# Performance work log

Hardware: AMD Instinct MI355X
Metric: run time of the kernel (lower is better)

Reference implementation:

```python
import jax, jax.numpy as jnp
import numpy as np

N = 96  # fixed by nn.LayerNorm([96]) in the module
EPS = 1e-6


def _dct2_matrix(n, dtype=jnp.float32):
    # DCT-II with the module's scaling (norm=None, returns 2*V):
    # D[k, i] = 2 * cos(pi * (2i + 1) * k / (2n))
    k = jnp.arange(n, dtype=dtype)[:, None]
    i = jnp.arange(n, dtype=dtype)[None, :]
    return 2.0 * jnp.cos(jnp.pi * (2.0 * i + 1.0) * k / (2.0 * n))


def _layernorm(y, gamma, beta):
    mu = jnp.mean(y, axis=-1, keepdims=True)
    var = jnp.mean(jnp.square(y - mu), axis=-1, keepdims=True)
    return (y - mu) * jax.lax.rsqrt(var + EPS) * gamma + beta


def setup_inputs() -> dict:
    key = jax.random.key(0)
    k1, k2, k3 = jax.random.split(key, 3)
    b, c, l = 512, 1024, N
    x = jax.random.normal(k1, (b, c, l), dtype=jnp.float32)
    # torch Linear default init ~ U(-1/sqrt(fan_in), 1/sqrt(fan_in)); gaussian*scale is fine for a baseline
    W1 = jax.random.normal(k2, (2 * N, N), dtype=jnp.float32) * (1.0 / np.sqrt(N))
    W2 = jax.random.normal(k3, (N, 2 * N), dtype=jnp.float32) * (1.0 / np.sqrt(2 * N))
    ln_gamma = jnp.ones((N,), dtype=jnp.float32)
    ln_beta = jnp.zeros((N,), dtype=jnp.float32)
    return {"x": x, "W1": W1, "W2": W2, "ln_gamma": ln_gamma, "ln_beta": ln_beta}


def reference(x, W1, W2, ln_gamma, ln_beta):
    # x: [b, c, 96]. The per-channel python loop in the original is just a
    # batched DCT-II along the last axis -> single matmul with the DCT matrix.
    D = _dct2_matrix(N, x.dtype)
    stack_dct = jnp.einsum('bcl,kl->bck', x, D)
    lr = _layernorm(stack_dct, ln_gamma, ln_beta)
    h = jax.nn.relu(jnp.einsum('bck,hk->bch', lr, W1))   # Linear(96 -> 192), dropout is identity in eval
    s = jax.nn.sigmoid(jnp.einsum('bch,kh->bck', h, W2))  # Linear(192 -> 96)
    lr_weight = _layernorm(s, ln_gamma, ln_beta)          # same LayerNorm module reused
    return x * lr_weight
```

## Files before the change

kernel.cpp:

```cpp
#include <hip/hip_runtime.h>
#include <math.h>

typedef _Float16 v8h  __attribute__((ext_vector_type(8)));
typedef float    fx4  __attribute__((ext_vector_type(4)));

#define S1_FRAGS 18
#define S2_FRAGS 36
#define S3_FRAGS 36

__global__ void prep_frags(const float* __restrict__ W1,
                           const float* __restrict__ W2,
                           v8h* __restrict__ ws) {
    const int f    = blockIdx.x;
    const int lane = threadIdx.x;
    v8h v;
    if (f < S1_FRAGS) {
        const int t = f / 3, s = f % 3;
        const int n  = t * 16 + (lane & 15);
        const int k0 = s * 32 + (lane >> 4) * 8;
#pragma unroll
        for (int j = 0; j < 8; ++j) {
            const int i = k0 + j;
            const float ang = 3.14159265358979323846f * (float)((2 * i + 1) * n) / 192.0f;
            v[j] = (_Float16)(2.0f * cosf(ang));
        }
    } else if (f < S1_FRAGS + S2_FRAGS) {
        const int g = f - S1_FRAGS;
        const int t = g / 3, s = g % 3;
        const int n  = t * 16 + (lane & 15);
        const int k0 = s * 32 + (lane >> 4) * 8;
#pragma unroll
        for (int j = 0; j < 8; ++j) v[j] = (_Float16)W1[n * 96 + k0 + j];
    } else {
        const int g = f - S1_FRAGS - S2_FRAGS;
        const int t = g / 6, s = g % 6;
        const int n  = t * 16 + (lane & 15);
        const int k0 = s * 32 + (lane >> 4) * 8;
#pragma unroll
        for (int j = 0; j < 8; ++j) v[j] = (_Float16)W2[n * 192 + k0 + j];
    }
    ws[f * 64 + lane] = v;
}

#define LDA 104
#define LDH 200

__global__ __launch_bounds__(256, 3)
void fused_dct_mlp(const float* __restrict__ x,
                   const float* __restrict__ gamma,
                   const float* __restrict__ beta,
                   const v8h* __restrict__ wf,
                   float* __restrict__ out) {
    __shared__ _Float16 LRB[64][LDA];
    __shared__ _Float16 HB[64][LDH];

    const int tid  = threadIdx.x;
    const int lane = tid & 63;
    const int wave = tid >> 6;
    const int m0   = wave * 16;
    const int lr_  = lane & 15;
    const int lk   = lane >> 4;

    const long row0 = (long)blockIdx.x * 64;
    const float* arow = x + (row0 + m0 + lr_) * 96;

    fx4 acc1[6];
#pragma unroll
    for (int t = 0; t < 6; ++t) acc1[t] = (fx4){0.f, 0.f, 0.f, 0.f};
#pragma unroll
    for (int s = 0; s < 3; ++s) {
        const float* ap = arow + s * 32 + lk * 8;
        fx4 a0 = *(const fx4*)ap;
        fx4 a1 = *(const fx4*)(ap + 4);
        v8h a;
#pragma unroll
        for (int j = 0; j < 4; ++j) { a[j] = (_Float16)a0[j]; a[4 + j] = (_Float16)a1[j]; }
#pragma unroll
        for (int t = 0; t < 6; ++t) {
            v8h b = wf[(t * 3 + s) * 64 + lane];
            acc1[t] = __builtin_amdgcn_mfma_f32_16x16x32_f16(a, b, acc1[t], 0, 0, 0);
        }
    }

    {
        float sum[4] = {0, 0, 0, 0}, sq[4] = {0, 0, 0, 0};
#pragma unroll
        for (int t = 0; t < 6; ++t)
#pragma unroll
            for (int r = 0; r < 4; ++r) { float v = acc1[t][r]; sum[r] += v; sq[r] += v * v; }
#pragma unroll
        for (int m = 1; m <= 8; m <<= 1)
#pragma unroll
            for (int r = 0; r < 4; ++r) {
                sum[r] += __shfl_xor(sum[r], m, 64);
                sq[r]  += __shfl_xor(sq[r],  m, 64);
            }
        float mu[4], rs[4];
#pragma unroll
        for (int r = 0; r < 4; ++r) {
            mu[r] = sum[r] * (1.0f / 96.0f);
            float var = sq[r] * (1.0f / 96.0f) - mu[r] * mu[r];
            rs[r] = rsqrtf(var + 1e-6f);
        }
#pragma unroll
        for (int t = 0; t < 6; ++t) {
            const int col = t * 16 + lr_;
            const float g = gamma[col], bb = beta[col];
#pragma unroll
            for (int r = 0; r < 4; ++r) {
                float w = (acc1[t][r] - mu[r]) * rs[r] * g + bb;
                LRB[m0 + lk * 4 + r][col] = (_Float16)w;
            }
        }
    }

    fx4 acc2[12];
#pragma unroll
    for (int t = 0; t < 12; ++t) acc2[t] = (fx4){0.f, 0.f, 0.f, 0.f};
#pragma unroll
    for (int s = 0; s < 3; ++s) {
        v8h a = *(const v8h*)&LRB[m0 + lr_][s * 32 + lk * 8];
        const v8h* bp = wf + S1_FRAGS * 64;
#pragma unroll
        for (int t = 0; t < 12; ++t) {
            v8h b = bp[(t * 3 + s) * 64 + lane];
            acc2[t] = __builtin_amdgcn_mfma_f32_16x16x32_f16(a, b, acc2[t], 0, 0, 0);
        }
    }
#pragma unroll
    for (int t = 0; t < 12; ++t) {
        const int col = t * 16 + lr_;
#pragma unroll
        for (int r = 0; r < 4; ++r)
            HB[m0 + lk * 4 + r][col] = (_Float16)fmaxf(acc2[t][r], 0.0f);
    }

    fx4 acc3[6];
#pragma unroll
    for (int t = 0; t < 6; ++t) acc3[t] = (fx4){0.f, 0.f, 0.f, 0.f};
#pragma unroll
    for (int s = 0; s < 6; ++s) {
        v8h a = *(const v8h*)&HB[m0 + lr_][s * 32 + lk * 8];
        const v8h* bp = wf + (S1_FRAGS + S2_FRAGS) * 64;
#pragma unroll
        for (int t = 0; t < 6; ++t) {
            v8h b = bp[(t * 6 + s) * 64 + lane];
            acc3[t] = __builtin_amdgcn_mfma_f32_16x16x32_f16(a, b, acc3[t], 0, 0, 0);
        }
    }
#pragma unroll
    for (int t = 0; t < 6; ++t)
#pragma unroll
        for (int r = 0; r < 4; ++r)
            acc3[t][r] = 1.0f / (1.0f + __expf(-acc3[t][r]));

    {
        float sum[4] = {0, 0, 0, 0}, sq[4] = {0, 0, 0, 0};
#pragma unroll
        for (int t = 0; t < 6; ++t)
#pragma unroll
            for (int r = 0; r < 4; ++r) { float v = acc3[t][r]; sum[r] += v; sq[r] += v * v; }
#pragma unroll
        for (int m = 1; m <= 8; m <<= 1)
#pragma unroll
            for (int r = 0; r < 4; ++r) {
                sum[r] += __shfl_xor(sum[r], m, 64);
                sq[r]  += __shfl_xor(sq[r],  m, 64);
            }
        float mu[4], rs[4];
#pragma unroll
        for (int r = 0; r < 4; ++r) {
            mu[r] = sum[r] * (1.0f / 96.0f);
            float var = sq[r] * (1.0f / 96.0f) - mu[r] * mu[r];
            rs[r] = rsqrtf(var + 1e-6f);
        }
#pragma unroll
        for (int t = 0; t < 6; ++t) {
            const int col = t * 16 + lr_;
            const float g = gamma[col], bb = beta[col];
#pragma unroll
            for (int r = 0; r < 4; ++r) {
                const long grow = row0 + m0 + lk * 4 + r;
                const long off  = grow * 96 + col;
                float w = (acc3[t][r] - mu[r]) * rs[r] * g + bb;
                out[off] = x[off] * w;
            }
        }
    }
}

extern "C" void kernel_launch(void* const* d_in, const int* in_sizes, int n_in,
                              void* d_out, int out_size, void* d_ws, size_t ws_size,
                              hipStream_t stream) {
    const float* x     = (const float*)d_in[0];
    const float* W1    = (const float*)d_in[1];
    const float* W2    = (const float*)d_in[2];
    const float* gamma = (const float*)d_in[3];
    const float* beta  = (const float*)d_in[4];
    float* out = (float*)d_out;
    v8h* ws = (v8h*)d_ws;

    prep_frags<<<S1_FRAGS + S2_FRAGS + S3_FRAGS, 64, 0, stream>>>(W1, W2, ws);

    const long rows = (long)in_sizes[0] / 96;
    fused_dct_mlp<<<(int)(rows / 64), 256, 0, stream>>>(x, gamma, beta, ws, out);
}
```

Baseline: 453.5 us.

## Transpose MFMA operands so each lane owns a row; vectorize LN and stores

Swaps the A/B operands of every MFMA so the accumulator holds the output transposed: each lane now owns one row and four consecutive columns. LayerNorm reductions then need only two cross-lane shuffles instead of eight per row set, and gamma/beta/x loads and the output store become 16-byte vector accesses. Shared memory is cut to one per-wave 16-row buffer reused for both intermediate stages, and launch bounds ask for 6 blocks per CU to raise occupancy. The risk is extra register pressure under the tighter bound and possible LDS bank conflicts on the 4-half writes.

```diff
diff --git a/kernel.cpp b/kernel.cpp
--- a/kernel.cpp
+++ b/kernel.cpp
@@ -2,6 +2,7 @@
 #include <math.h>
 
 typedef _Float16 v8h  __attribute__((ext_vector_type(8)));
+typedef _Float16 h4   __attribute__((ext_vector_type(4)));
 typedef float    fx4  __attribute__((ext_vector_type(4)));
 
 #define S1_FRAGS 18
@@ -44,73 +45,72 @@
 
 #define LDA 104
 #define LDH 200
+#define CHUNK (16 * LDH)
 
-__global__ __launch_bounds__(256, 3)
+__global__ __launch_bounds__(256, 6)
 void fused_dct_mlp(const float* __restrict__ x,
                    const float* __restrict__ gamma,
                    const float* __restrict__ beta,
                    const v8h* __restrict__ wf,
                    float* __restrict__ out) {
-    __shared__ _Float16 LRB[64][LDA];
-    __shared__ _Float16 HB[64][LDH];
+    __shared__ __align__(16) _Float16 BUF[4][CHUNK];
 
     const int tid  = threadIdx.x;
     const int lane = tid & 63;
     const int wave = tid >> 6;
-    const int m0   = wave * 16;
     const int lr_  = lane & 15;
     const int lk   = lane >> 4;
 
-    const long row0 = (long)blockIdx.x * 64;
-    const float* arow = x + (row0 + m0 + lr_) * 96;
+    _Float16* const base = &BUF[wave][0];
+    const long row  = (long)blockIdx.x * 64 + wave * 16 + lr_;
+    const float* arow = x + row * 96;
+
+    fx4 xa[6];
+#pragma unroll
+    for (int s = 0; s < 3; ++s) {
+        const float* ap = arow + s * 32 + lk * 8;
+        xa[2 * s]     = *(const fx4*)ap;
+        xa[2 * s + 1] = *(const fx4*)(ap + 4);
+    }
+    v8h xf[3];
+#pragma unroll
+    for (int s = 0; s < 3; ++s)
+#pragma unroll
+        for (int j = 0; j < 4; ++j) {
+            xf[s][j]     = (_Float16)xa[2 * s][j];
+            xf[s][4 + j] = (_Float16)xa[2 * s + 1][j];
+        }
 
     fx4 acc1[6];
 #pragma unroll
     for (int t = 0; t < 6; ++t) acc1[t] = (fx4){0.f, 0.f, 0.f, 0.f};
 #pragma unroll
-    for (int s = 0; s < 3; ++s) {
-        const float* ap = arow + s * 32 + lk * 8;
-        fx4 a0 = *(const fx4*)ap;
-        fx4 a1 = *(const fx4*)(ap + 4);
-        v8h a;
+    for (int s = 0; s < 3; ++s)
 #pragma unroll
-        for (int j = 0; j < 4; ++j) { a[j] = (_Float16)a0[j]; a[4 + j] = (_Float16)a1[j]; }
-#pragma unroll
-        for (int t = 0; t < 6; ++t) {
-            v8h b = wf[(t * 3 + s) * 64 + lane];
-            acc1[t] = __builtin_amdgcn_mfma_f32_16x16x32_f16(a, b, acc1[t], 0, 0, 0);
-        }
-    }
+        for (int t = 0; t < 6; ++t)
+            acc1[t] = __builtin_amdgcn_mfma_f32_16x16x32_f16(
+                wf[(t * 3 + s) * 64 + lane], xf[s], acc1[t], 0, 0, 0);
 
     {
-        float sum[4] = {0, 0, 0, 0}, sq[4] = {0, 0, 0, 0};
+        float sum = 0.f, sq = 0.f;
 #pragma unroll
         for (int t = 0; t < 6; ++t)
 #pragma unroll
-            for (int r = 0; r < 4; ++r) { float v = acc1[t][r]; sum[r] += v; sq[r] += v * v; }
-#pragma unroll
-        for (int m = 1; m <= 8; m <<= 1)
-#pragma unroll
-            for (int r = 0; r < 4; ++r) {
-                sum[r] += __shfl_xor(sum[r], m, 64);
-                sq[r]  += __shfl_xor(sq[r],  m, 64);
-            }
-        float mu[4], rs[4];
-#pragma unroll
-        for (int r = 0; r < 4; ++r) {
-            mu[r] = sum[r] * (1.0f / 96.0f);
-            float var = sq[r] * (1.0f / 96.0f) - mu[r] * mu[r];
-            rs[r] = rsqrtf(var + 1e-6f);
-        }
+            for (int r = 0; r < 4; ++r) { float v = acc1[t][r]; sum += v; sq += v * v; }
+        sum += __shfl_xor(sum, 16); sq += __shfl_xor(sq, 16);
+        sum += __shfl_xor(sum, 32); sq += __shfl_xor(sq, 32);
+        const float mu = sum * (1.0f / 96.0f);
+        const float rs = rsqrtf(sq * (1.0f / 96.0f) - mu * mu + 1e-6f);
 #pragma unroll
         for (int t = 0; t < 6; ++t) {
-            const int col = t * 16 + lr_;
-            const float g = gamma[col], bb = beta[col];
+            const int c0 = t * 16 + lk * 4;
+            const fx4 g  = *(const fx4*)(gamma + c0);
+            const fx4 bb = *(const fx4*)(beta + c0);
+            h4 p;
 #pragma unroll
-            for (int r = 0; r < 4; ++r) {
-                float w = (acc1[t][r] - mu[r]) * rs[r] * g + bb;
-                LRB[m0 + lk * 4 + r][col] = (_Float16)w;
-            }
+            for (int r = 0; r < 4; ++r)
+                p[r] = (_Float16)((acc1[t][r] - mu) * rs * g[r] + bb[r]);
+            *(h4*)(base + lr_ * LDA + c0) = p;
         }
     }
 
@@ -119,20 +119,19 @@
     for (int t = 0; t < 12; ++t) acc2[t] = (fx4){0.f, 0.f, 0.f, 0.f};
 #pragma unroll
     for (int s = 0; s < 3; ++s) {
-        v8h a = *(const v8h*)&LRB[m0 + lr_][s * 32 + lk * 8];
+        const v8h af = *(const v8h*)(base + lr_ * LDA + s * 32 + lk * 8);
         const v8h* bp = wf + S1_FRAGS * 64;
 #pragma unroll
-        for (int t = 0; t < 12; ++t) {
-            v8h b = bp[(t * 3 + s) * 64 + lane];
-            acc2[t] = __builtin_amdgcn_mfma_f32_16x16x32_f16(a, b, acc2[t], 0, 0, 0);
-        }
+        for (int t = 0; t < 12; ++t)
+            acc2[t] = __builtin_amdgcn_mfma_f32_16x16x32_f16(
+                bp[(t * 3 + s) * 64 + lane], af, acc2[t], 0, 0, 0);
     }
 #pragma unroll
     for (int t = 0; t < 12; ++t) {
-        const int col = t * 16 + lr_;
+        h4 p;
 #pragma unroll
-        for (int r = 0; r < 4; ++r)
-            HB[m0 + lk * 4 + r][col] = (_Float16)fmaxf(acc2[t][r], 0.0f);
+        for (int r = 0; r < 4; ++r) p[r] = (_Float16)fmaxf(acc2[t][r], 0.0f);
+        *(h4*)(base + lr_ * LDH + t * 16 + lk * 4) = p;
     }
 
     fx4 acc3[6];
@@ -140,13 +139,12 @@
     for (int t = 0; t < 6; ++t) acc3[t] = (fx4){0.f, 0.f, 0.f, 0.f};
 #pragma unroll
     for (int s = 0; s < 6; ++s) {
-        v8h a = *(const v8h*)&HB[m0 + lr_][s * 32 + lk * 8];
+        const v8h hf = *(const v8h*)(base + lr_ * LDH + s * 32 + lk * 8);
         const v8h* bp = wf + (S1_FRAGS + S2_FRAGS) * 64;
 #pragma unroll
-        for (int t = 0; t < 6; ++t) {
-            v8h b = bp[(t * 6 + s) * 64 + lane];
-            acc3[t] = __builtin_amdgcn_mfma_f32_16x16x32_f16(a, b, acc3[t], 0, 0, 0);
-        }
+        for (int t = 0; t < 6; ++t)
+            acc3[t] = __builtin_amdgcn_mfma_f32_16x16x32_f16(
+                bp[(t * 6 + s) * 64 + lane], hf, acc3[t], 0, 0, 0);
     }
 #pragma unroll
     for (int t = 0; t < 6; ++t)
@@ -155,36 +153,26 @@
             acc3[t][r] = 1.0f / (1.0f + __expf(-acc3[t][r]));
 
     {
-        float sum[4] = {0, 0, 0, 0}, sq[4] = {0, 0, 0, 0};
+        float sum = 0.f, sq = 0.f;
 #pragma unroll
         for (int t = 0; t < 6; ++t)
 #pragma unroll
-            for (int r = 0; r < 4; ++r) { float v = acc3[t][r]; sum[r] += v; sq[r] += v * v; }
-#pragma unroll
-        for (int m = 1; m <= 8; m <<= 1)
-#pragma unroll
-            for (int r = 0; r < 4; ++r) {
-                sum[r] += __shfl_xor(sum[r], m, 64);
-                sq[r]  += __shfl_xor(sq[r],  m, 64);
-            }
-        float mu[4], rs[4];
-#pragma unroll
-        for (int r = 0; r < 4; ++r) {
-            mu[r] = sum[r] * (1.0f / 96.0f);
-            float var = sq[r] * (1.0f / 96.0f) - mu[r] * mu[r];
-            rs[r] = rsqrtf(var + 1e-6f);
-        }
+            for (int r = 0; r < 4; ++r) { float v = acc3[t][r]; sum += v; sq += v * v; }
+        sum += __shfl_xor(sum, 16); sq += __shfl_xor(sq, 16);
+        sum += __shfl_xor(sum, 32); sq += __shfl_xor(sq, 32);
+        const float mu = sum * (1.0f / 96.0f);
+        const float rs = rsqrtf(sq * (1.0f / 96.0f) - mu * mu + 1e-6f);
 #pragma unroll
         for (int t = 0; t < 6; ++t) {
-            const int col = t * 16 + lr_;
-            const float g = gamma[col], bb = beta[col];
+            const int c0 = t * 16 + lk * 4;
+            const fx4 g  = *(const fx4*)(gamma + c0);
+            const fx4 bb = *(const fx4*)(beta + c0);
+            const fx4 xv = *(const fx4*)(arow + c0);
+            fx4 o;
 #pragma unroll
-            for (int r = 0; r < 4; ++r) {
-                const long grow = row0 + m0 + lk * 4 + r;
-                const long off  = grow * 96 + col;
-                float w = (acc3[t][r] - mu[r]) * rs[r] * g + bb;
-                out[off] = x[off] * w;
-            }
+            for (int r = 0; r < 4; ++r)
+                o[r] = xv[r] * ((acc3[t][r] - mu) * rs * g[r] + bb[r]);
+            *(fx4*)(out + row * 96 + c0) = o;
         }
     }
 }
```

Result: slower. 582.3 us (+28.4%).
